# Performance work log

Hardware: AMD Instinct MI355X
Metric: run time of the kernel (lower is better)

Reference implementation:

```python
import jax, jax.numpy as jnp
import numpy as np
import math

B, S, D, H = 2, 2048, 4096, 32
HD = D // H          # 128 head dim
HALF = HD // 2       # 64 rotary pairs
AL = 10              # adapter length


def setup_inputs() -> dict:
    key = jax.random.key(0)
    ks = jax.random.split(key, 8)
    sc = 0.02
    x = jax.random.normal(ks[0], (B, S, D), jnp.float32)
    adapter = jax.random.normal(ks[1], (B, AL, D), jnp.float32)
    wq = jax.random.normal(ks[2], (D, D), jnp.float32) * sc
    wk = jax.random.normal(ks[3], (D, D), jnp.float32) * sc
    wv = jax.random.normal(ks[4], (D, D), jnp.float32) * sc
    wo = jax.random.normal(ks[5], (D, D), jnp.float32) * sc
    gate = jax.random.normal(ks[6], (1, H, 1, 1), jnp.float32) * 0.1
    # rotary frequencies (LLaMA convention), freqs_cis = exp(i * t * f)
    inv_freq = 1.0 / (10000.0 ** (np.arange(0, HD, 2).astype(np.float32) / HD))
    ang = np.outer(np.arange(S, dtype=np.float32), inv_freq)  # [S, HALF]
    cos = jnp.asarray(np.cos(ang), jnp.float32)
    sin = jnp.asarray(np.sin(ang), jnp.float32)
    # additive causal mask [1,1,S,S]
    mask = jnp.triu(jnp.full((S, S), -1e9, jnp.float32), 1)[None, None]
    return {"x": x, "mask": mask, "cos": cos, "sin": sin, "wq": wq,
            "wk": wk, "wv": wv, "wo": wo, "gate": gate,
            "adapter": adapter, "start_pos": 0}


def _rope(t, cos, sin):
    # t: [B,S,H,HD]; complex rotate consecutive pairs
    tr = t.reshape(*t.shape[:-1], HALF, 2)
    t0, t1 = tr[..., 0], tr[..., 1]
    c = cos[None, :, None, :]  # [1,S,1,HALF]
    s = sin[None, :, None, :]
    r0 = t0 * c - t1 * s
    r1 = t0 * s + t1 * c
    return jnp.stack([r0, r1], axis=-1).reshape(t.shape)


def reference(x, mask, cos, sin, wq, wk, wv, wo, gate, adapter, start_pos):
    bsz, seqlen, _ = x.shape
    scale = 1.0 / math.sqrt(HD)
    xq = (x @ wq.T).reshape(bsz, seqlen, H, HD)
    xk = (x @ wk.T).reshape(bsz, seqlen, H, HD)
    xv = (x @ wv.T).reshape(bsz, seqlen, H, HD)
    xq = _rope(xq, cos, sin)
    xk = _rope(xk, cos, sin)
    # training path: keys/values = current tokens (start_pos == 0)
    q = xq.transpose(0, 2, 1, 3)   # [B,H,S,HD]
    k = xk.transpose(0, 2, 1, 3)
    v = xv.transpose(0, 2, 1, 3)
    scores = jnp.einsum('bhqd,bhkd->bhqk', q, k) * scale + mask
    scores = jax.nn.softmax(scores.astype(jnp.float32), axis=-1).astype(x.dtype)
    out = jnp.einsum('bhqk,bhkd->bhqd', scores, v)
    # gated adapter cross-attention (adapter_len > 1 branch)
    a_len = adapter.shape[1]
    a_v = (adapter @ wv.T).reshape(bsz, a_len, H, HD).transpose(0, 2, 1, 3)
    a_k = (adapter @ wk.T).reshape(bsz, a_len, H, HD).transpose(0, 2, 1, 3)
    a_scores = jnp.einsum('bhqd,bhkd->bhqk', q, a_k) * scale
    a_scores = jnp.tanh(gate) * jax.nn.softmax(
        a_scores.astype(jnp.float32), axis=-1).astype(x.dtype)
    out = out + jnp.einsum('bhqk,bhkd->bhqd', a_scores, a_v)
    out = out.transpose(0, 2, 1, 3).reshape(bsz, seqlen, -1)
    return out @ wo.T
```

## Files before the change

### kernel.cpp

```cpp
#include <hip/hip_runtime.h>
#include <hip/hip_bf16.h>
#include <stdint.h>

#define B_ 2
#define S_ 2048
#define D_ 4096
#define H_ 32
#define HD_ 128
#define HALF_ 64
#define AL_ 10
#define MROWS (B_*S_)

typedef __hip_bfloat16 bf16;
typedef __attribute__((ext_vector_type(8))) __bf16 bf16x8;
typedef __attribute__((ext_vector_type(4))) float f32x4;
typedef __attribute__((ext_vector_type(4))) unsigned short us4;

__device__ __forceinline__ void gld_lds16(const void* g, void* l) {
    __builtin_amdgcn_global_load_lds((const __attribute__((address_space(1))) void*)g,
                                     (__attribute__((address_space(3))) void*)l, 16, 0, 0);
}

__global__ void detect_dtype(const unsigned short* __restrict__ x, int* __restrict__ flag) {
    __shared__ int cnt;
    if (threadIdx.x == 0) cnt = 0;
    __syncthreads();
    int bad = 0;
#pragma unroll
    for (int i = 0; i < 16; i++) {
        unsigned int u = x[threadIdx.x * 16 + i];
        float v = __uint_as_float(u << 16);
        if (!(fabsf(v) < 1000.f)) bad++;
    }
    atomicAdd(&cnt, bad);
    __syncthreads();
    if (threadIdx.x == 0) flag[0] = (cnt > 64) ? 1 : 0;
}

__global__ void convert_bf16(const void* __restrict__ in, bf16* __restrict__ out,
                             const int* __restrict__ flag, int n) {
    int i = (blockIdx.x * 256 + threadIdx.x) * 4;
    if (i >= n) return;
    if (flag[0]) {
        float4 f = *(const float4*)((const float*)in + i);
        out[i + 0] = __float2bfloat16(f.x);
        out[i + 1] = __float2bfloat16(f.y);
        out[i + 2] = __float2bfloat16(f.z);
        out[i + 3] = __float2bfloat16(f.w);
    } else {
        *(us4*)(out + i) = *(const us4*)((const unsigned short*)in + i);
    }
}

template<int MODE>
__global__ __launch_bounds__(256) void gemm_bt(
    const bf16* __restrict__ A, const bf16* __restrict__ W,
    const bf16* __restrict__ cosb, const bf16* __restrict__ sinb,
    void* __restrict__ outv, const int* __restrict__ flag, int K)
{
    __shared__ __align__(16) bf16 sA[128*64];
    __shared__ __align__(16) bf16 sB[128*64];
    const int tid  = threadIdx.x;
    const int wave = tid >> 6, lane = tid & 63;
    const int quad = lane >> 4, col = lane & 15;
    const int m0 = blockIdx.y * 128, n0 = blockIdx.x * 128;
    const int wm = (wave >> 1) * 64, wn = (wave & 1) * 64;

    bool f32o = false;
    if (MODE == 2) f32o = (flag[0] != 0);

    f32x4 acc[4][4];
#pragma unroll
    for (int i = 0; i < 4; i++)
#pragma unroll
        for (int j = 0; j < 4; j++) acc[i][j] = {0.f, 0.f, 0.f, 0.f};

    for (int k0 = 0; k0 < K; k0 += 64) {
        __syncthreads();
#pragma unroll
        for (int i = 0; i < 4; i++) {
            int c   = i * 256 + tid;
            int row = c >> 3;
            int cc  = (c & 7) ^ (row & 7);
            gld_lds16(A + (size_t)(m0 + row) * K + k0 + cc * 8,
                      sA + (size_t)(i * 256 + wave * 64) * 8);
            gld_lds16(W + (size_t)(n0 + row) * K + k0 + cc * 8,
                      sB + (size_t)(i * 256 + wave * 64) * 8);
        }
        __syncthreads();

#pragma unroll
        for (int kk = 0; kk < 64; kk += 32) {
            bf16x8 af[4], bfr[4];
#pragma unroll
            for (int mt = 0; mt < 4; mt++) {
                int r  = wm + mt * 16 + col;
                int ck = ((kk >> 3) + quad) ^ (r & 7);
                af[mt] = *(const bf16x8*)(sA + r * 64 + ck * 8);
            }
#pragma unroll
            for (int nt = 0; nt < 4; nt++) {
                int r  = wn + nt * 16 + col;
                int ck = ((kk >> 3) + quad) ^ (r & 7);
                bfr[nt] = *(const bf16x8*)(sB + r * 64 + ck * 8);
            }
#pragma unroll
            for (int mt = 0; mt < 4; mt++)
#pragma unroll
                for (int nt = 0; nt < 4; nt++)
                    acc[mt][nt] = __builtin_amdgcn_mfma_f32_16x16x32_bf16(
                        af[mt], bfr[nt], acc[mt][nt], 0, 0, 0);
        }
    }

#pragma unroll
    for (int mt = 0; mt < 4; mt++) {
#pragma unroll
        for (int nt = 0; nt < 4; nt++) {
            int n = n0 + wn + nt * 16 + col;
#pragma unroll
            for (int e = 0; e < 4; e++) {
                int m   = m0 + wm + mt * 16 + quad * 4 + e;
                float v = acc[mt][nt][e];
                if (MODE == 2) {
                    if (f32o) ((float*)outv)[(size_t)m * D_ + n] = v;
                    else      ((bf16*)outv)[(size_t)m * D_ + n] = __float2bfloat16(v);
                } else {
                    int b = m >> 11, s = m & (S_ - 1);
                    int h = n >> 7,  hd = n & (HD_ - 1);
                    bf16* out = (bf16*)outv;
                    if (MODE == 0) {
                        float other = __shfl_xor(v, 1);
                        float c  = __bfloat162float(cosb[s * HALF_ + (hd >> 1)]);
                        float sn = __bfloat162float(sinb[s * HALF_ + (hd >> 1)]);
                        float r  = (hd & 1) ? (v * c + other * sn)
                                            : (v * c - other * sn);
                        out[((size_t)(b * H_ + h) * S_ + s) * HD_ + hd] = __float2bfloat16(r);
                    } else {
                        out[((size_t)(b * H_ + h) * HD_ + hd) * S_ + s] = __float2bfloat16(v);
                    }
                }
            }
        }
    }
}

__global__ __launch_bounds__(256) void attn_fwd(
    const bf16* __restrict__ q, const bf16* __restrict__ k,
    const bf16* __restrict__ vT, bf16* __restrict__ o)
{
    __shared__ __align__(16) bf16 sQ[64*128];
    __shared__ __align__(16) bf16 sK[64*128];
    __shared__ __align__(16) bf16 sV[128*64];
    __shared__ __align__(16) bf16 sP[64*64];

    const int tid  = threadIdx.x, wave = tid >> 6, lane = tid & 63;
    const int quad = lane >> 4, col = lane & 15;
    const int qt = blockIdx.x, bh = blockIdx.y;
    const int q0 = qt * 64;
    const bf16* qb = q  + (size_t)bh * S_ * HD_;
    const bf16* kb = k  + (size_t)bh * S_ * HD_;
    const bf16* vb = vT + (size_t)bh * HD_ * S_;

#pragma unroll
    for (int i = 0; i < 4; i++) {
        int c = i * 256 + tid;
        int row = c >> 4;
        int cc  = (c & 15) ^ (row & 7);
        gld_lds16(qb + (size_t)(q0 + row) * HD_ + cc * 8,
                  sQ + (size_t)(i * 256 + wave * 64) * 8);
    }

    float mst[4], lst[4];
#pragma unroll
    for (int e = 0; e < 4; e++) { mst[e] = -1e30f; lst[e] = 0.f; }
    f32x4 oacc[8];
#pragma unroll
    for (int i = 0; i < 8; i++) oacc[i] = {0.f, 0.f, 0.f, 0.f};

    const float scale = 0.08838834764831845f;

    for (int kt = 0; kt <= qt; kt++) {
        const int k0 = kt * 64;
        __syncthreads();
#pragma unroll
        for (int i = 0; i < 4; i++) {
            int c = i * 256 + tid;
            int rowK = c >> 4, ccK = (c & 15) ^ (rowK & 7);
            gld_lds16(kb + (size_t)(k0 + rowK) * HD_ + ccK * 8,
                      sK + (size_t)(i * 256 + wave * 64) * 8);
            int rowV = c >> 3, ccV = (c & 7) ^ (rowV & 7);
            gld_lds16(vb + (size_t)rowV * S_ + k0 + ccV * 8,
                      sV + (size_t)(i * 256 + wave * 64) * 8);
        }
        __syncthreads();

        f32x4 sc[4];
#pragma unroll
        for (int nt = 0; nt < 4; nt++) sc[nt] = {0.f, 0.f, 0.f, 0.f};
#pragma unroll
        for (int kk = 0; kk < 128; kk += 32) {
            int rq  = wave * 16 + col;
            int ckq = ((kk >> 3) + quad) ^ (rq & 7);
            bf16x8 aq = *(const bf16x8*)(sQ + rq * 128 + ckq * 8);
#pragma unroll
            for (int nt = 0; nt < 4; nt++) {
                int rk  = nt * 16 + col;
                int ckk = ((kk >> 3) + quad) ^ (rk & 7);
                bf16x8 bk = *(const bf16x8*)(sK + rk * 128 + ckk * 8);
                sc[nt] = __builtin_amdgcn_mfma_f32_16x16x32_bf16(aq, bk, sc[nt], 0, 0, 0);
            }
        }

        const bool diag = (kt == qt);
#pragma unroll
        for (int nt = 0; nt < 4; nt++)
#pragma unroll
            for (int e = 0; e < 4; e++) {
                float v = sc[nt][e] * scale;
                if (diag && (nt * 16 + col > wave * 16 + quad * 4 + e)) v = -1e30f;
                sc[nt][e] = v;
            }

        float alpha_[4];
#pragma unroll
        for (int e = 0; e < 4; e++) {
            float mx = fmaxf(fmaxf(sc[0][e], sc[1][e]), fmaxf(sc[2][e], sc[3][e]));
#pragma unroll
            for (int off = 1; off < 16; off <<= 1) mx = fmaxf(mx, __shfl_xor(mx, off));
            float mnew = fmaxf(mst[e], mx);
            float al   = __expf(mst[e] - mnew);
            float rs   = 0.f;
            int prow = wave * 16 + quad * 4 + e;
#pragma unroll
            for (int nt = 0; nt < 4; nt++) {
                float p = __expf(sc[nt][e] - mnew);
                rs += p;
                int pcol = nt * 16 + col;
                int pc   = (pcol >> 3) ^ (prow & 7);
                sP[prow * 64 + pc * 8 + (pcol & 7)] = __float2bfloat16(p);
            }
#pragma unroll
            for (int off = 1; off < 16; off <<= 1) rs += __shfl_xor(rs, off);
            lst[e] = lst[e] * al + rs;
            mst[e] = mnew;
            alpha_[e] = al;
        }
#pragma unroll
        for (int nt = 0; nt < 8; nt++)
#pragma unroll
            for (int e = 0; e < 4; e++) oacc[nt][e] *= alpha_[e];
        __syncthreads();

#pragma unroll
        for (int kk = 0; kk < 64; kk += 32) {
            int rp  = wave * 16 + col;
            int ckp = ((kk >> 3) + quad) ^ (rp & 7);
            bf16x8 pf = *(const bf16x8*)(sP + rp * 64 + ckp * 8);
#pragma unroll
            for (int nt = 0; nt < 8; nt++) {
                int rv  = nt * 16 + col;
                int ckv = ((kk >> 3) + quad) ^ (rv & 7);
                bf16x8 vf = *(const bf16x8*)(sV + rv * 64 + ckv * 8);
                oacc[nt] = __builtin_amdgcn_mfma_f32_16x16x32_bf16(pf, vf, oacc[nt], 0, 0, 0);
            }
        }
    }

    const int b = bh >> 5, h = bh & (H_ - 1);
#pragma unroll
    for (int e = 0; e < 4; e++) {
        int s = q0 + wave * 16 + quad * 4 + e;
        float inv = 1.f / lst[e];
#pragma unroll
        for (int nt = 0; nt < 8; nt++) {
            int hd = nt * 16 + col;
            o[((size_t)(b * S_ + s) * H_ + h) * HD_ + hd] =
                __float2bfloat16(oacc[nt][e] * inv);
        }
    }
}

__global__ __launch_bounds__(256) void adapter_kv(
    const bf16* __restrict__ adp, const bf16* __restrict__ wk,
    const bf16* __restrict__ wv, float* __restrict__ ak, float* __restrict__ av)
{
    const int tid = threadIdx.x, wave = tid >> 6, lane = tid & 63;
    const int gid = blockIdx.x * 4 + wave;
    const int n = gid & (D_ - 1), b = gid >> 12;
    const bf16* w    = blockIdx.y ? wv : wk;
    float*      outp = blockIdx.y ? av : ak;

    float acc[AL_];
#pragma unroll
    for (int j = 0; j < AL_; j++) acc[j] = 0.f;

    for (int t = 0; t < 8; t++) {
        int kb = t * 512 + lane * 8;
        bf16x8 w8 = *(const bf16x8*)(w + (size_t)n * D_ + kb);
        float wf[8];
#pragma unroll
        for (int i = 0; i < 8; i++) wf[i] = (float)w8[i];
#pragma unroll
        for (int j = 0; j < AL_; j++) {
            bf16x8 a8 = *(const bf16x8*)(adp + (size_t)(b * AL_ + j) * D_ + kb);
            float s = 0.f;
#pragma unroll
            for (int i = 0; i < 8; i++) s += (float)a8[i] * wf[i];
            acc[j] += s;
        }
    }
#pragma unroll
    for (int j = 0; j < AL_; j++) {
        float v = acc[j];
#pragma unroll
        for (int off = 1; off < 64; off <<= 1) v += __shfl_xor(v, off);
        if (lane == 0) outp[(size_t)(b * AL_ + j) * D_ + n] = v;
    }
}

__global__ __launch_bounds__(256) void adapter_add(
    const bf16* __restrict__ q, const float* __restrict__ ak,
    const float* __restrict__ av, const bf16* __restrict__ gate,
    bf16* __restrict__ o)
{
    const int tid = threadIdx.x, wave = tid >> 6, lane = tid & 63;
    const int g = blockIdx.x * 4 + wave;
    const int s = g & (S_ - 1);
    const int h = (g >> 11) & (H_ - 1);
    const int b = g >> 16;
    const int hd = lane * 2;

    const bf16* qp = q + ((size_t)(b * H_ + h) * S_ + s) * HD_ + hd;
    float q0f = __bfloat162float(qp[0]);
    float q1f = __bfloat162float(qp[1]);
    const float scale = 0.08838834764831845f;

    float sc[AL_];
#pragma unroll
    for (int j = 0; j < AL_; j++) {
        const float* akp = ak + (size_t)(b * AL_ + j) * D_ + h * HD_ + hd;
        float p = q0f * akp[0] + q1f * akp[1];
#pragma unroll
        for (int off = 1; off < 64; off <<= 1) p += __shfl_xor(p, off);
        sc[j] = p * scale;
    }
    float mx = sc[0];
#pragma unroll
    for (int j = 1; j < AL_; j++) mx = fmaxf(mx, sc[j]);
    float sum = 0.f;
#pragma unroll
    for (int j = 0; j < AL_; j++) { sc[j] = __expf(sc[j] - mx); sum += sc[j]; }
    float wgt = tanhf(__bfloat162float(gate[h])) / sum;

    float a0 = 0.f, a1 = 0.f;
#pragma unroll
    for (int j = 0; j < AL_; j++) {
        const float* avp = av + (size_t)(b * AL_ + j) * D_ + h * HD_ + hd;
        a0 += sc[j] * avp[0];
        a1 += sc[j] * avp[1];
    }
    bf16* op = o + ((size_t)(b * S_ + s) * H_ + h) * HD_ + hd;
    op[0] = __float2bfloat16(__bfloat162float(op[0]) + wgt * a0);
    op[1] = __float2bfloat16(__bfloat162float(op[1]) + wgt * a1);
}

extern "C" void kernel_launch(void* const* d_in, const int* in_sizes, int n_in,
                              void* d_out, int out_size, void* d_ws, size_t ws_size,
                              hipStream_t stream)
{
    const void* x_raw    = d_in[0];
    const void* cos_raw  = d_in[2];
    const void* sin_raw  = d_in[3];
    const void* wq_raw   = d_in[4];
    const void* wk_raw   = d_in[5];
    const void* wv_raw   = d_in[6];
    const void* wo_raw   = d_in[7];
    const void* gate_raw = d_in[8];
    const void* adp_raw  = d_in[9];

    const size_t NE = (size_t)B_ * S_ * D_;
    const int    CS = S_ * HALF_;
    const int    AD = B_ * AL_ * D_;

    bf16* xc   = (bf16*)d_ws;
    bf16* wqc  = xc  + NE;
    bf16* wkc  = wqc + NE;
    bf16* wvc  = wkc + NE;
    bf16* woc  = wvc + NE;
    bf16* qb   = woc + NE;
    bf16* kb   = qb  + NE;
    bf16* vb   = kb  + NE;
    bf16* cosc = vb  + NE;
    bf16* sinc = cosc + CS;
    bf16* adpc = sinc + CS;
    bf16* gatec= adpc + AD;
    float* akb = (float*)(gatec + 32);
    float* avb = akb + AD;
    int*  flag = (int*)(avb + AD);
    bf16* ab   = xc;

    dim3 blk(256);
    detect_dtype<<<1, 256, 0, stream>>>((const unsigned short*)x_raw, flag);

    convert_bf16<<<dim3((int)(NE/4 + 255) / 256), blk, 0, stream>>>(x_raw,  xc,  flag, (int)NE);
    convert_bf16<<<dim3((int)(NE/4 + 255) / 256), blk, 0, stream>>>(wq_raw, wqc, flag, (int)NE);
    convert_bf16<<<dim3((int)(NE/4 + 255) / 256), blk, 0, stream>>>(wk_raw, wkc, flag, (int)NE);
    convert_bf16<<<dim3((int)(NE/4 + 255) / 256), blk, 0, stream>>>(wv_raw, wvc, flag, (int)NE);
    convert_bf16<<<dim3((int)(NE/4 + 255) / 256), blk, 0, stream>>>(wo_raw, woc, flag, (int)NE);
    convert_bf16<<<dim3((CS/4 + 255) / 256), blk, 0, stream>>>(cos_raw,  cosc, flag, CS);
    convert_bf16<<<dim3((CS/4 + 255) / 256), blk, 0, stream>>>(sin_raw,  sinc, flag, CS);
    convert_bf16<<<dim3((AD/4 + 255) / 256), blk, 0, stream>>>(adp_raw,  adpc, flag, AD);
    convert_bf16<<<dim3(1), blk, 0, stream>>>(gate_raw, gatec, flag, 32);

    dim3 gg(D_ / 128, MROWS / 128);
    gemm_bt<0><<<gg, blk, 0, stream>>>(xc, wqc, cosc, sinc, qb, flag, D_);
    gemm_bt<0><<<gg, blk, 0, stream>>>(xc, wkc, cosc, sinc, kb, flag, D_);
    gemm_bt<1><<<gg, blk, 0, stream>>>(xc, wvc, cosc, sinc, vb, flag, D_);
    adapter_kv<<<dim3(2048, 2), blk, 0, stream>>>(adpc, wkc, wvc, akb, avb);
    attn_fwd<<<dim3(S_ / 64, B_ * H_), blk, 0, stream>>>(qb, kb, vb, ab);
    adapter_add<<<dim3(B_ * H_ * S_ / 4), blk, 0, stream>>>(qb, akb, avb, gatec, ab);
    gemm_bt<2><<<gg, blk, 0, stream>>>(ab, woc, cosc, sinc, d_out, flag, D_);
}
```

Measured before the change: 1.507 ms.

## Enlarge attention query tile to 128 rows with register-resident Q fragments

The flash-attention kernel now processes 128 query rows per block, with each wave owning 32 rows. Q fragments are loaded once into registers, each K/V tile is reused across twice as many queries, and the Q shared-memory buffer is aliased with K/V/P. Blocks are launched heaviest-first (reversed qt) to improve causal load balance, and one barrier per iteration is removed. The cost is higher register pressure, which launch_bounds(256,2) tries to contain, and half as many blocks.

```diff
diff --git a/kernel.cpp b/kernel.cpp
--- a/kernel.cpp
+++ b/kernel.cpp
@@ -145,42 +145,60 @@
     }
 }
 
-__global__ __launch_bounds__(256) void attn_fwd(
+__global__ __launch_bounds__(256, 2) void attn_fwd(
     const bf16* __restrict__ q, const bf16* __restrict__ k,
     const bf16* __restrict__ vT, bf16* __restrict__ o)
 {
-    __shared__ __align__(16) bf16 sQ[64*128];
-    __shared__ __align__(16) bf16 sK[64*128];
-    __shared__ __align__(16) bf16 sV[128*64];
-    __shared__ __align__(16) bf16 sP[64*64];
+    __shared__ __align__(16) bf16 smem[24576];
+    bf16* sK = smem;
+    bf16* sV = smem + 8192;
+    bf16* sP = smem + 16384;
 
     const int tid  = threadIdx.x, wave = tid >> 6, lane = tid & 63;
     const int quad = lane >> 4, col = lane & 15;
-    const int qt = blockIdx.x, bh = blockIdx.y;
-    const int q0 = qt * 64;
+    const int qt = (gridDim.x - 1) - blockIdx.x;
+    const int bh = blockIdx.y;
+    const int q0 = qt * 128;
     const bf16* qb = q  + (size_t)bh * S_ * HD_;
     const bf16* kb = k  + (size_t)bh * S_ * HD_;
     const bf16* vb = vT + (size_t)bh * HD_ * S_;
 
 #pragma unroll
-    for (int i = 0; i < 4; i++) {
+    for (int i = 0; i < 8; i++) {
         int c = i * 256 + tid;
         int row = c >> 4;
         int cc  = (c & 15) ^ (row & 7);
         gld_lds16(qb + (size_t)(q0 + row) * HD_ + cc * 8,
-                  sQ + (size_t)(i * 256 + wave * 64) * 8);
-    }
-
-    float mst[4], lst[4];
-#pragma unroll
-    for (int e = 0; e < 4; e++) { mst[e] = -1e30f; lst[e] = 0.f; }
-    f32x4 oacc[8];
-#pragma unroll
-    for (int i = 0; i < 8; i++) oacc[i] = {0.f, 0.f, 0.f, 0.f};
+                  smem + (size_t)(i * 256 + wave * 64) * 8);
+    }
+    __syncthreads();
+
+    bf16x8 qf[2][4];
+#pragma unroll
+    for (int rq = 0; rq < 2; rq++) {
+        int row = wave * 32 + rq * 16 + col;
+#pragma unroll
+        for (int kkI = 0; kkI < 4; kkI++) {
+            int ck = (kkI * 4 + quad) ^ (row & 7);
+            qf[rq][kkI] = *(const bf16x8*)(smem + row * 128 + ck * 8);
+        }
+    }
+
+    float mst[2][4], lst[2][4];
+#pragma unroll
+    for (int rq = 0; rq < 2; rq++)
+#pragma unroll
+        for (int e = 0; e < 4; e++) { mst[rq][e] = -1e30f; lst[rq][e] = 0.f; }
+    f32x4 oacc[2][8];
+#pragma unroll
+    for (int rq = 0; rq < 2; rq++)
+#pragma unroll
+        for (int i = 0; i < 8; i++) oacc[rq][i] = {0.f, 0.f, 0.f, 0.f};
 
     const float scale = 0.08838834764831845f;
-
-    for (int kt = 0; kt <= qt; kt++) {
+    const int ktEnd = 2 * qt + 2;
+
+    for (int kt = 0; kt < ktEnd; kt++) {
         const int k0 = kt * 64;
         __syncthreads();
 #pragma unroll
@@ -195,90 +213,104 @@
         }
         __syncthreads();
 
-        f32x4 sc[4];
-#pragma unroll
-        for (int nt = 0; nt < 4; nt++) sc[nt] = {0.f, 0.f, 0.f, 0.f};
-#pragma unroll
-        for (int kk = 0; kk < 128; kk += 32) {
-            int rq  = wave * 16 + col;
-            int ckq = ((kk >> 3) + quad) ^ (rq & 7);
-            bf16x8 aq = *(const bf16x8*)(sQ + rq * 128 + ckq * 8);
+        f32x4 sc[2][4];
+#pragma unroll
+        for (int rq = 0; rq < 2; rq++)
+#pragma unroll
+            for (int nt = 0; nt < 4; nt++) sc[rq][nt] = {0.f, 0.f, 0.f, 0.f};
+#pragma unroll
+        for (int kkI = 0; kkI < 4; kkI++) {
 #pragma unroll
             for (int nt = 0; nt < 4; nt++) {
                 int rk  = nt * 16 + col;
-                int ckk = ((kk >> 3) + quad) ^ (rk & 7);
+                int ckk = (kkI * 4 + quad) ^ (rk & 7);
                 bf16x8 bk = *(const bf16x8*)(sK + rk * 128 + ckk * 8);
-                sc[nt] = __builtin_amdgcn_mfma_f32_16x16x32_bf16(aq, bk, sc[nt], 0, 0, 0);
-            }
-        }
-
-        const bool diag = (kt == qt);
-#pragma unroll
-        for (int nt = 0; nt < 4; nt++)
+                sc[0][nt] = __builtin_amdgcn_mfma_f32_16x16x32_bf16(qf[0][kkI], bk, sc[0][nt], 0, 0, 0);
+                sc[1][nt] = __builtin_amdgcn_mfma_f32_16x16x32_bf16(qf[1][kkI], bk, sc[1][nt], 0, 0, 0);
+            }
+        }
+
+        const bool diag = (kt >= 2 * qt);
+#pragma unroll
+        for (int rq = 0; rq < 2; rq++)
+#pragma unroll
+            for (int nt = 0; nt < 4; nt++)
+#pragma unroll
+                for (int e = 0; e < 4; e++) {
+                    float v = sc[rq][nt][e] * scale;
+                    if (diag && (k0 + nt * 16 + col > q0 + wave * 32 + rq * 16 + quad * 4 + e))
+                        v = -1e30f;
+                    sc[rq][nt][e] = v;
+                }
+
+        float alpha_[2][4];
+#pragma unroll
+        for (int rq = 0; rq < 2; rq++)
 #pragma unroll
             for (int e = 0; e < 4; e++) {
-                float v = sc[nt][e] * scale;
-                if (diag && (nt * 16 + col > wave * 16 + quad * 4 + e)) v = -1e30f;
-                sc[nt][e] = v;
-            }
-
-        float alpha_[4];
-#pragma unroll
-        for (int e = 0; e < 4; e++) {
-            float mx = fmaxf(fmaxf(sc[0][e], sc[1][e]), fmaxf(sc[2][e], sc[3][e]));
-#pragma unroll
-            for (int off = 1; off < 16; off <<= 1) mx = fmaxf(mx, __shfl_xor(mx, off));
-            float mnew = fmaxf(mst[e], mx);
-            float al   = __expf(mst[e] - mnew);
-            float rs   = 0.f;
-            int prow = wave * 16 + quad * 4 + e;
-#pragma unroll
-            for (int nt = 0; nt < 4; nt++) {
-                float p = __expf(sc[nt][e] - mnew);
-                rs += p;
-                int pcol = nt * 16 + col;
-                int pc   = (pcol >> 3) ^ (prow & 7);
-                sP[prow * 64 + pc * 8 + (pcol & 7)] = __float2bfloat16(p);
-            }
-#pragma unroll
-            for (int off = 1; off < 16; off <<= 1) rs += __shfl_xor(rs, off);
-            lst[e] = lst[e] * al + rs;
-            mst[e] = mnew;
-            alpha_[e] = al;
-        }
-#pragma unroll
-        for (int nt = 0; nt < 8; nt++)
-#pragma unroll
-            for (int e = 0; e < 4; e++) oacc[nt][e] *= alpha_[e];
-        __syncthreads();
-
-#pragma unroll
-        for (int kk = 0; kk < 64; kk += 32) {
-            int rp  = wave * 16 + col;
-            int ckp = ((kk >> 3) + quad) ^ (rp & 7);
-            bf16x8 pf = *(const bf16x8*)(sP + rp * 64 + ckp * 8);
+                float mx = fmaxf(fmaxf(sc[rq][0][e], sc[rq][1][e]),
+                                 fmaxf(sc[rq][2][e], sc[rq][3][e]));
+#pragma unroll
+                for (int off = 1; off < 16; off <<= 1) mx = fmaxf(mx, __shfl_xor(mx, off));
+                float mnew = fmaxf(mst[rq][e], mx);
+                float al   = __expf(mst[rq][e] - mnew);
+                float rs   = 0.f;
+                int prow = wave * 32 + rq * 16 + quad * 4 + e;
+#pragma unroll
+                for (int nt = 0; nt < 4; nt++) {
+                    float p = __expf(sc[rq][nt][e] - mnew);
+                    rs += p;
+                    int pcol = nt * 16 + col;
+                    int pc   = (pcol >> 3) ^ (prow & 7);
+                    sP[prow * 64 + pc * 8 + (pcol & 7)] = __float2bfloat16(p);
+                }
+#pragma unroll
+                for (int off = 1; off < 16; off <<= 1) rs += __shfl_xor(rs, off);
+                lst[rq][e] = lst[rq][e] * al + rs;
+                mst[rq][e] = mnew;
+                alpha_[rq][e] = al;
+            }
+#pragma unroll
+        for (int rq = 0; rq < 2; rq++)
+#pragma unroll
+            for (int nt = 0; nt < 8; nt++)
+#pragma unroll
+                for (int e = 0; e < 4; e++) oacc[rq][nt][e] *= alpha_[rq][e];
+
+#pragma unroll
+        for (int kkI = 0; kkI < 2; kkI++) {
+            bf16x8 pf[2];
+#pragma unroll
+            for (int rq = 0; rq < 2; rq++) {
+                int rp  = wave * 32 + rq * 16 + col;
+                int ckp = (kkI * 4 + quad) ^ (rp & 7);
+                pf[rq] = *(const bf16x8*)(sP + rp * 64 + ckp * 8);
+            }
 #pragma unroll
             for (int nt = 0; nt < 8; nt++) {
                 int rv  = nt * 16 + col;
-                int ckv = ((kk >> 3) + quad) ^ (rv & 7);
+                int ckv = (kkI * 4 + quad) ^ (rv & 7);
                 bf16x8 vf = *(const bf16x8*)(sV + rv * 64 + ckv * 8);
-                oacc[nt] = __builtin_amdgcn_mfma_f32_16x16x32_bf16(pf, vf, oacc[nt], 0, 0, 0);
+                oacc[0][nt] = __builtin_amdgcn_mfma_f32_16x16x32_bf16(pf[0], vf, oacc[0][nt], 0, 0, 0);
+                oacc[1][nt] = __builtin_amdgcn_mfma_f32_16x16x32_bf16(pf[1], vf, oacc[1][nt], 0, 0, 0);
             }
         }
     }
 
     const int b = bh >> 5, h = bh & (H_ - 1);
 #pragma unroll
-    for (int e = 0; e < 4; e++) {
-        int s = q0 + wave * 16 + quad * 4 + e;
-        float inv = 1.f / lst[e];
-#pragma unroll
-        for (int nt = 0; nt < 8; nt++) {
-            int hd = nt * 16 + col;
-            o[((size_t)(b * S_ + s) * H_ + h) * HD_ + hd] =
-                __float2bfloat16(oacc[nt][e] * inv);
-        }
-    }
+    for (int rq = 0; rq < 2; rq++)
+#pragma unroll
+        for (int e = 0; e < 4; e++) {
+            int s = q0 + wave * 32 + rq * 16 + quad * 4 + e;
+            float inv = 1.f / lst[rq][e];
+#pragma unroll
+            for (int nt = 0; nt < 8; nt++) {
+                int hd = nt * 16 + col;
+                o[((size_t)(b * S_ + s) * H_ + h) * HD_ + hd] =
+                    __float2bfloat16(oacc[rq][nt][e] * inv);
+            }
+        }
 }
 
 __global__ __launch_bounds__(256) void adapter_kv(
@@ -418,7 +450,7 @@
     gemm_bt<0><<<gg, blk, 0, stream>>>(xc, wkc, cosc, sinc, kb, flag, D_);
     gemm_bt<1><<<gg, blk, 0, stream>>>(xc, wvc, cosc, sinc, vb, flag, D_);
     adapter_kv<<<dim3(2048, 2), blk, 0, stream>>>(adpc, wkc, wvc, akb, avb);
-    attn_fwd<<<dim3(S_ / 64, B_ * H_), blk, 0, stream>>>(qb, kb, vb, ab);
+    attn_fwd<<<dim3(S_ / 128, B_ * H_), blk, 0, stream>>>(qb, kb, vb, ab);
     adapter_add<<<dim3(B_ * H_ * S_ / 4), blk, 0, stream>>>(qb, akb, avb, gatec, ab);
     gemm_bt<2><<<gg, blk, 0, stream>>>(ab, woc, cosc, sinc, d_out, flag, D_);
 }
```

Result: no change. 1.501 ms (-0.4%).
